# Optimization experiments

Hardware: AMD Instinct MI355X
Metric: run time of the kernel (lower is better)

## Reference

```python
import jax, jax.numpy as jnp
import numpy as np
from jax import lax

B, N, C = 8, 4096, 512
NH, R = 8, 8
HD = C // NH
EPS = 1e-3  # keras LayerNormalization default epsilon


def setup_inputs() -> dict:
    key = jax.random.key(0)
    ks = jax.random.split(key, 8)
    s = 0.02
    x = jax.random.normal(ks[0], (B, N, C), dtype=jnp.float32)
    Wq = jax.random.normal(ks[1], (C, C), dtype=jnp.float32) * s
    Wkv = jax.random.normal(ks[2], (C, 2 * C), dtype=jnp.float32) * s
    conv_w = jax.random.normal(ks[3], (R, R, C, C), dtype=jnp.float32) * s  # HWIO
    gamma = jnp.ones((C,), dtype=jnp.float32)
    beta = jnp.zeros((C,), dtype=jnp.float32)
    Wp = jax.random.normal(ks[4], (C, C), dtype=jnp.float32) * s
    bp = jnp.zeros((C,), dtype=jnp.float32)
    return {"x": x, "Wq": Wq, "Wkv": Wkv, "conv_w": conv_w,
            "gamma": gamma, "beta": beta, "Wp": Wp, "bp": bp}


def reference(x, Wq, Wkv, conv_w, gamma, beta, Wp, bp):
    b, n, c = x.shape
    h = w = int(np.sqrt(n))
    scale = 1.0 / np.sqrt(float(HD))

    # queries: Rearrange 'b n (hd nh) -> b n nh hd' then 'b n nh hd -> b nh n hd'
    q = x @ Wq                                   # [B, N, C]
    q = q.reshape(b, n, HD, NH).transpose(0, 3, 1, 2)  # [B, NH, N, HD]

    # spatial reduction of K/V: strided conv (SAME) + layernorm
    fmap = x.reshape(b, h, w, c)
    fmap = lax.conv_general_dilated(
        fmap, conv_w, window_strides=(R, R), padding="SAME",
        dimension_numbers=("NHWC", "HWIO", "NHWC"))   # [B, h/R, w/R, C]
    m = fmap.shape[1] * fmap.shape[2]
    fmap = fmap.reshape(b, m, c)
    mu = jnp.mean(fmap, axis=-1, keepdims=True)
    var = jnp.var(fmap, axis=-1, keepdims=True)
    fmap = (fmap - mu) * lax.rsqrt(var + EPS) * gamma + beta

    # key/value: Rearrange 'b m (f nh hd) -> b m f nh hd', perm [2,0,3,1,4]
    kv = fmap @ Wkv                              # [B, M, 2C]
    kv = kv.reshape(b, m, 2, NH, HD).transpose(2, 0, 3, 1, 4)  # [2, B, NH, M, HD]
    k, v = kv[0], kv[1]

    attn = jax.nn.softmax(jnp.einsum("bhnd,bhmd->bhnm", q, k) * scale, axis=-1)
    out = jnp.einsum("bhnm,bhmd->bhnd", attn, v)  # [B, NH, N, HD]
    out = out.transpose(0, 2, 1, 3).reshape(b, n, c)  # 'b n h c -> b n (h c)'
    return out @ Wp + bp
```

## Files before the change

### kernel.cpp

```cpp
#include <hip/hip_runtime.h>

typedef unsigned short u16;
typedef __bf16 bf16x8 __attribute__((ext_vector_type(8)));
typedef float floatx4 __attribute__((ext_vector_type(4)));

__device__ __forceinline__ u16 f2bf(float f) {
    unsigned u = __float_as_uint(f);
    u += 0x7fff + ((u >> 16) & 1);
    return (u16)(u >> 16);
}

#define GLOAD_LDS16(g, l) __builtin_amdgcn_global_load_lds( \
    (const __attribute__((address_space(1))) void*)(g),      \
    (__attribute__((address_space(3))) void*)(l), 16, 0, 0)

#define WCONV_STRIDE 32832

__global__ __launch_bounds__(256) void cast_x_kernel(
    const float* __restrict__ x, u16* __restrict__ x_bf)
{
    const int tid = threadIdx.x;
    const size_t base = (size_t)blockIdx.x * 1024 + tid;
    const float4* src = (const float4*)x;
    uint4* dst = (uint4*)x_bf;
    float4 a[4], b[4];
    #pragma unroll
    for (int i = 0; i < 4; ++i) {
        a[i] = src[(base + i * 256) * 2];
        b[i] = src[(base + i * 256) * 2 + 1];
    }
    #pragma unroll
    for (int i = 0; i < 4; ++i) {
        uint4 o;
        o.x = (unsigned)f2bf(a[i].x) | ((unsigned)f2bf(a[i].y) << 16);
        o.y = (unsigned)f2bf(a[i].z) | ((unsigned)f2bf(a[i].w) << 16);
        o.z = (unsigned)f2bf(b[i].x) | ((unsigned)f2bf(b[i].y) << 16);
        o.w = (unsigned)f2bf(b[i].z) | ((unsigned)f2bf(b[i].w) << 16);
        dst[base + i * 256] = o;
    }
}

__global__ __launch_bounds__(256) void prep2_kernel(
    const float* __restrict__ conv_w, u16* __restrict__ WconvT,
    const float* __restrict__ Wq, u16* __restrict__ WqTp,
    const float* __restrict__ Wp, u16* __restrict__ WpT,
    const float* __restrict__ Wkv, u16* __restrict__ WkvT)
{
    int blk = blockIdx.x;
    const int tid = threadIdx.x;
    __shared__ __align__(16) char smem[16896];

    if (blk < 2048) {
        u16 (*T)[66] = (u16(*)[66])smem;
        const int by = blk >> 8;
        const int bx = blk & 255;
        const int c0 = by * 64, k0 = bx * 128;
        const int f = tid & 15, kl = tid >> 4;
        #pragma unroll
        for (int it = 0; it < 8; ++it) {
            int k = kl + it * 16;
            float4 v = *(const float4*)(conv_w + (size_t)(k0 + k) * 512 + c0 + f * 4);
            *(unsigned*)&T[k][f * 4]     = (unsigned)f2bf(v.x) | ((unsigned)f2bf(v.y) << 16);
            *(unsigned*)&T[k][f * 4 + 2] = (unsigned)f2bf(v.z) | ((unsigned)f2bf(v.w) << 16);
        }
        __syncthreads();
        const int cl = tid >> 6, p = tid & 63;
        #pragma unroll
        for (int it = 0; it < 16; ++it) {
            int c = cl + it * 4;
            unsigned lo = T[p * 2][c], hi = T[p * 2 + 1][c];
            *(unsigned*)&WconvT[(size_t)(c0 + c) * WCONV_STRIDE + k0 + p * 2] = lo | (hi << 16);
        }
        return;
    }
    blk -= 2048;

    const float* in; u16* outp; int R, Cn, bx, by; bool perm = false;
    if (blk < 256)      { in = Wq;  outp = WqTp; R = 512; Cn = 512;  bx = blk & 15; by = blk >> 4; perm = true; }
    else if (blk < 512) { blk -= 256; in = Wp;  outp = WpT;  R = 512; Cn = 512;  bx = blk & 15; by = blk >> 4; }
    else                { blk -= 512; in = Wkv; outp = WkvT; R = 512; Cn = 1024; bx = blk & 31; by = blk >> 5; }
    float (*tile)[33] = (float(*)[33])smem;
    const int c0 = bx * 32, r0 = by * 32;
    const int tx = tid & 31, ty = tid >> 5;
    #pragma unroll
    for (int yy = 0; yy < 4; ++yy)
        tile[ty + yy * 8][tx] = in[(size_t)(r0 + ty + yy * 8) * Cn + c0 + tx];
    __syncthreads();
    #pragma unroll
    for (int yy = 0; yy < 4; ++yy) {
        int cc = c0 + ty + yy * 8;
        int np = perm ? ((cc & 7) * 64 + (cc >> 3)) : cc;
        outp[(size_t)np * R + r0 + tx] = f2bf(tile[tx][ty + yy * 8]);
    }
}

template<int MODE, int ASRC>
__global__ __launch_bounds__(256) void gemm_bt(
    const u16* __restrict__ A, const u16* __restrict__ B, float* __restrict__ out,
    int M, int N, int K, int BS, int KC, const float* __restrict__ bias)
{
    __shared__ u16 As[2][128 * 32];
    __shared__ u16 Bs[2][128 * 32];
    const int tid = threadIdx.x;
    const int wv = tid >> 6, lane = tid & 63;
    const int quad = lane >> 4, l15 = lane & 15;

    constexpr int GX = (MODE == 2) ? 8 : 4;
    int id = blockIdx.y * GX + blockIdx.x;
    if (MODE != 0) {
        const int nwg = GX * gridDim.y;
        id = (id & 7) * (nwg >> 3) + (id >> 3);
    }
    const int bm = (id / GX) * 128, bn = (id % GX) * 128;
    const int k0 = blockIdx.z * KC;
    const int wr = wv >> 1, wc = wv & 1;

    floatx4 acc[4][4];
    #pragma unroll
    for (int i = 0; i < 4; ++i)
        #pragma unroll
        for (int j = 0; j < 4; ++j)
            acc[i][j] = (floatx4){0.f, 0.f, 0.f, 0.f};

    for (int kt = 0; kt < KC; kt += 64) {
        const int kk = k0 + kt;
        #pragma unroll
        for (int hf = 0; hf < 2; ++hf) {
            #pragma unroll
            for (int c2 = 0; c2 < 2; ++c2) {
                int idx = ((wv * 2 + c2) * 64 + lane) * 8;
                int row = idx >> 5, col = idx & 31;
                int k = kk + hf * 32 + col;
                if (ASRC == 0) {
                    const u16* ga = A + (size_t)(bm + row) * K + k;
                    GLOAD_LDS16(ga, &As[hf][(wv * 2 + c2) * 512]);
                } else {
                    int p = bm + row;
                    int b = p >> 6, ij = p & 63, ii = ij >> 3, jj = ij & 7;
                    int r12 = k >> 9, r1 = r12 >> 3, r2 = r12 & 7;
                    int n = (ii * 8 + r1) * 64 + jj * 8 + r2;
                    const u16* ga = A + ((size_t)(b * 4096 + n)) * 512 + (k & 511);
                    GLOAD_LDS16(ga, &As[hf][(wv * 2 + c2) * 512]);
                }
                const u16* gb = B + (size_t)(bn + row) * BS + k;
                GLOAD_LDS16(gb, &Bs[hf][(wv * 2 + c2) * 512]);
            }
        }
        __syncthreads();
        #pragma unroll
        for (int ks = 0; ks < 2; ++ks) {
            bf16x8 af[4], bfr[4];
            #pragma unroll
            for (int i = 0; i < 4; ++i)
                af[i] = *(const bf16x8*)&As[ks][(wr * 64 + i * 16 + l15) * 32 + quad * 8];
            #pragma unroll
            for (int j = 0; j < 4; ++j)
                bfr[j] = *(const bf16x8*)&Bs[ks][(wc * 64 + j * 16 + l15) * 32 + quad * 8];
            #pragma unroll
            for (int i = 0; i < 4; ++i)
                #pragma unroll
                for (int j = 0; j < 4; ++j)
                    acc[i][j] = __builtin_amdgcn_mfma_f32_16x16x32_bf16(af[i], bfr[j], acc[i][j], 0, 0, 0);
        }
        __syncthreads();
    }

    #pragma unroll
    for (int i = 0; i < 4; ++i) {
        #pragma unroll
        for (int j = 0; j < 4; ++j) {
            #pragma unroll
            for (int r = 0; r < 4; ++r) {
                int m = bm + wr * 64 + i * 16 + quad * 4 + r;
                int n = bn + wc * 64 + j * 16 + l15;
                float v = acc[i][j][r];
                if (MODE == 0) {
                    ((u16*)out)[(size_t)blockIdx.z * 262144 + (size_t)m * N + n] = f2bf(v);
                } else if (MODE == 1) {
                    int b = m >> 12, nn = m & 4095;
                    int h = n >> 6, d = n & 63;
                    ((u16*)out)[((size_t)((b * 8 + h) * 4096 + nn)) * 64 + d] = f2bf(v);
                } else if (MODE == 2) {
                    int b = m >> 6, mm = m & 63;
                    int f = n >> 9, c = n & 511, h = c >> 6, d = c & 63;
                    size_t idx;
                    if (f == 0) idx = ((size_t)((b * 8 + h) * 64 + mm)) * 64 + d;
                    else        idx = 262144 + ((size_t)((b * 8 + h) * 64 + d)) * 64 + mm;
                    out[idx] = v;
                } else {
                    out[(size_t)m * 512 + n] = v + bias[n];
                }
            }
        }
    }
}

__global__ __launch_bounds__(256) void reduce_ln_bf16(
    const u16* __restrict__ part, u16* __restrict__ out,
    const float* __restrict__ gamma, const float* __restrict__ beta)
{
    int row = blockIdx.x, tid = threadIdx.x;
    const unsigned* base = (const unsigned*)(part + (size_t)row * 512) + tid;
    float2 v = {0.f, 0.f};
    #pragma unroll 8
    for (int z = 0; z < 32; ++z) {
        unsigned u = base[(size_t)z * 131072];
        v.x += __uint_as_float(u << 16);
        v.y += __uint_as_float(u & 0xffff0000u);
    }
    float s = v.x + v.y, ss = v.x * v.x + v.y * v.y;
    #pragma unroll
    for (int off = 32; off > 0; off >>= 1) {
        s  += __shfl_down(s, off);
        ss += __shfl_down(ss, off);
    }
    __shared__ float red[8];
    __shared__ float stats[2];
    int wvi = tid >> 6, lane = tid & 63;
    if (lane == 0) { red[wvi * 2] = s; red[wvi * 2 + 1] = ss; }
    __syncthreads();
    if (tid == 0) {
        float S = red[0] + red[2] + red[4] + red[6];
        float SS = red[1] + red[3] + red[5] + red[7];
        float mean = S * (1.f / 512.f);
        float var = SS * (1.f / 512.f) - mean * mean;
        stats[0] = mean; stats[1] = rsqrtf(var + 1e-3f);
    }
    __syncthreads();
    float mean = stats[0], rstd = stats[1];
    float o0 = (v.x - mean) * rstd * gamma[tid * 2]     + beta[tid * 2];
    float o1 = (v.y - mean) * rstd * gamma[tid * 2 + 1] + beta[tid * 2 + 1];
    unsigned w = (unsigned)f2bf(o0) | ((unsigned)f2bf(o1) << 16);
    *(unsigned*)&out[(size_t)row * 512 + tid * 2] = w;
}

__global__ __launch_bounds__(256) void attn_mfma(
    const u16* __restrict__ qbf, const float* __restrict__ kvf, u16* __restrict__ attn_out)
{
    __shared__ u16 Ksh[64 * 64];
    __shared__ u16 Vt[64 * 64];
    __shared__ u16 Psh[4][32 * 64];
    const int bh = blockIdx.x, qt = blockIdx.y;
    const int tid = threadIdx.x;
    const int wv = tid >> 6, lane = tid & 63;
    const int quad = lane >> 4, l15 = lane & 15;

    {
        const float* kb = kvf + (size_t)bh * 4096;
        const float* vb = kvf + 262144 + (size_t)bh * 4096;
        for (int t = tid; t < 2048; t += 256) {
            float2 a = ((const float2*)kb)[t];
            ((unsigned*)Ksh)[t] = (unsigned)f2bf(a.x) | ((unsigned)f2bf(a.y) << 16);
            float2 b2 = ((const float2*)vb)[t];
            ((unsigned*)Vt)[t] = (unsigned)f2bf(b2.x) | ((unsigned)f2bf(b2.y) << 16);
        }
    }
    __syncthreads();

    const u16* qb = qbf + ((size_t)bh * 4096 + qt * 128 + wv * 32) * 64;
    bf16x8 qf[2][2];
    #pragma unroll
    for (int i = 0; i < 2; ++i)
        #pragma unroll
        for (int ks = 0; ks < 2; ++ks)
            qf[i][ks] = *(const bf16x8*)(qb + (i * 16 + l15) * 64 + ks * 32 + quad * 8);

    floatx4 s[2][4];
    #pragma unroll
    for (int i = 0; i < 2; ++i)
        #pragma unroll
        for (int j = 0; j < 4; ++j)
            s[i][j] = (floatx4){0.f, 0.f, 0.f, 0.f};
    #pragma unroll
    for (int j = 0; j < 4; ++j) {
        #pragma unroll
        for (int ks = 0; ks < 2; ++ks) {
            bf16x8 kf = *(const bf16x8*)&Ksh[(j * 16 + l15) * 64 + ks * 32 + quad * 8];
            #pragma unroll
            for (int i = 0; i < 2; ++i)
                s[i][j] = __builtin_amdgcn_mfma_f32_16x16x32_bf16(qf[i][ks], kf, s[i][j], 0, 0, 0);
        }
    }

    u16* P = Psh[wv];
    float rs[2][4];
    #pragma unroll
    for (int i = 0; i < 2; ++i)
        #pragma unroll
        for (int r = 0; r < 4; ++r) rs[i][r] = 0.f;
    #pragma unroll
    for (int i = 0; i < 2; ++i)
        #pragma unroll
        for (int j = 0; j < 4; ++j)
            #pragma unroll
            for (int r = 0; r < 4; ++r) {
                float e = __expf(s[i][j][r] * 0.125f);
                rs[i][r] += e;
                P[(i * 16 + quad * 4 + r) * 64 + j * 16 + l15] = f2bf(e);
            }
    #pragma unroll
    for (int m = 1; m < 16; m <<= 1)
        #pragma unroll
        for (int i = 0; i < 2; ++i)
            #pragma unroll
            for (int r = 0; r < 4; ++r)
                rs[i][r] += __shfl_xor(rs[i][r], m);
    __syncthreads();

    floatx4 o[2][4];
    #pragma unroll
    for (int i = 0; i < 2; ++i)
        #pragma unroll
        for (int j = 0; j < 4; ++j)
            o[i][j] = (floatx4){0.f, 0.f, 0.f, 0.f};
    #pragma unroll
    for (int ks = 0; ks < 2; ++ks) {
        bf16x8 pf[2];
        #pragma unroll
        for (int i = 0; i < 2; ++i)
            pf[i] = *(const bf16x8*)&P[(i * 16 + l15) * 64 + ks * 32 + quad * 8];
        #pragma unroll
        for (int j = 0; j < 4; ++j) {
            bf16x8 vf = *(const bf16x8*)&Vt[(j * 16 + l15) * 64 + ks * 32 + quad * 8];
            #pragma unroll
            for (int i = 0; i < 2; ++i)
                o[i][j] = __builtin_amdgcn_mfma_f32_16x16x32_bf16(pf[i], vf, o[i][j], 0, 0, 0);
        }
    }

    const int b = bh >> 3, h = bh & 7;
    #pragma unroll
    for (int i = 0; i < 2; ++i) {
        #pragma unroll
        for (int r = 0; r < 4; ++r) {
            float inv = 1.f / rs[i][r];
            int n = qt * 128 + wv * 32 + i * 16 + quad * 4 + r;
            u16* op = attn_out + ((size_t)(b * 4096 + n)) * 512 + h * 64;
            #pragma unroll
            for (int j = 0; j < 4; ++j)
                op[j * 16 + l15] = f2bf(o[i][j][r] * inv);
        }
    }
}

extern "C" void kernel_launch(void* const* d_in, const int* in_sizes, int n_in,
                              void* d_out, int out_size, void* d_ws, size_t ws_size,
                              hipStream_t stream) {
    const float* x      = (const float*)d_in[0];
    const float* Wq     = (const float*)d_in[1];
    const float* Wkv    = (const float*)d_in[2];
    const float* conv_w = (const float*)d_in[3];
    const float* gamma  = (const float*)d_in[4];
    const float* beta   = (const float*)d_in[5];
    const float* Wp     = (const float*)d_in[6];
    const float* bp     = (const float*)d_in[7];
    float* out = (float*)d_out;

    char* w = (char*)d_ws;
    const size_t MB = 1ull << 20;
    u16*   x_bf      = (u16*)(w + 0);
    u16*   WconvT    = (u16*)(w + 32 * MB);
    u16*   WqTp      = (u16*)(w + 66 * MB);
    u16*   WkvT      = (u16*)(w + 67 * MB);
    u16*   WpT       = (u16*)(w + 68 * MB);
    u16*   q_bf      = (u16*)(w + 69 * MB);
    u16*   fmap_part = (u16*)(w + 101 * MB);
    u16*   fmap_ln   = (u16*)(w + 117 * MB);
    float* kv_f      = (float*)(w + 118 * MB);
    u16*   attn_bf   = (u16*)(w + 120 * MB);

    cast_x_kernel<<<2048, 256, 0, stream>>>(x, x_bf);
    prep2_kernel<<<3072, 256, 0, stream>>>(conv_w, WconvT, Wq, WqTp, Wp, WpT, Wkv, WkvT);

    gemm_bt<1, 0><<<dim3(4, 256, 1), 256, 0, stream>>>(x_bf, WqTp, (float*)q_bf, 32768, 512, 512, 512, 512, nullptr);
    gemm_bt<0, 1><<<dim3(4, 4, 32), 256, 0, stream>>>(x_bf, WconvT, (float*)fmap_part, 512, 512, 32768, WCONV_STRIDE, 1024, nullptr);
    reduce_ln_bf16<<<512, 256, 0, stream>>>(fmap_part, fmap_ln, gamma, beta);
    gemm_bt<2, 0><<<dim3(8, 4, 1), 256, 0, stream>>>(fmap_ln, WkvT, kv_f, 512, 1024, 512, 512, 512, nullptr);
    attn_mfma<<<dim3(64, 32), 256, 0, stream>>>(q_bf, kv_f, attn_bf);
    gemm_bt<3, 0><<<dim3(4, 256, 1), 256, 0, stream>>>(attn_bf, WpT, out, 32768, 512, 512, 512, 512, bp);
}
```

Measured before the change: 317.4 us.

## Merge prep kernels, co-launch Q and conv GEMMs, double-buffer GEMM K loop

Folds the x cast into the weight-prep kernel so it is one launch. The Q-projection GEMM and the strided-conv split-K GEMM now run as one fused launch with a block-index dispatch. The GEMM body now uses a ping-pong double-buffered 32-wide K loop, so global-to-LDS loads for the next step overlap the MFMA compute on the current one. This removes launch gaps and tail underutilisation, at the cost of finer-grained syncs and more complex block scheduling.

```diff
diff --git a/kernel.cpp b/kernel.cpp
--- a/kernel.cpp
+++ b/kernel.cpp
@@ -16,31 +16,8 @@
 
 #define WCONV_STRIDE 32832
 
-__global__ __launch_bounds__(256) void cast_x_kernel(
-    const float* __restrict__ x, u16* __restrict__ x_bf)
-{
-    const int tid = threadIdx.x;
-    const size_t base = (size_t)blockIdx.x * 1024 + tid;
-    const float4* src = (const float4*)x;
-    uint4* dst = (uint4*)x_bf;
-    float4 a[4], b[4];
-    #pragma unroll
-    for (int i = 0; i < 4; ++i) {
-        a[i] = src[(base + i * 256) * 2];
-        b[i] = src[(base + i * 256) * 2 + 1];
-    }
-    #pragma unroll
-    for (int i = 0; i < 4; ++i) {
-        uint4 o;
-        o.x = (unsigned)f2bf(a[i].x) | ((unsigned)f2bf(a[i].y) << 16);
-        o.y = (unsigned)f2bf(a[i].z) | ((unsigned)f2bf(a[i].w) << 16);
-        o.z = (unsigned)f2bf(b[i].x) | ((unsigned)f2bf(b[i].y) << 16);
-        o.w = (unsigned)f2bf(b[i].z) | ((unsigned)f2bf(b[i].w) << 16);
-        dst[base + i * 256] = o;
-    }
-}
-
-__global__ __launch_bounds__(256) void prep2_kernel(
+__global__ __launch_bounds__(256) void prep_kernel(
+    const float* __restrict__ x, u16* __restrict__ x_bf,
     const float* __restrict__ conv_w, u16* __restrict__ WconvT,
     const float* __restrict__ Wq, u16* __restrict__ WqTp,
     const float* __restrict__ Wp, u16* __restrict__ WpT,
@@ -48,6 +25,30 @@
 {
     int blk = blockIdx.x;
     const int tid = threadIdx.x;
+
+    if (blk < 2048) {
+        const size_t base = (size_t)blk * 1024 + tid;
+        const float4* src = (const float4*)x;
+        uint4* dst = (uint4*)x_bf;
+        float4 a[4], b[4];
+        #pragma unroll
+        for (int i = 0; i < 4; ++i) {
+            a[i] = src[(base + i * 256) * 2];
+            b[i] = src[(base + i * 256) * 2 + 1];
+        }
+        #pragma unroll
+        for (int i = 0; i < 4; ++i) {
+            uint4 o;
+            o.x = (unsigned)f2bf(a[i].x) | ((unsigned)f2bf(a[i].y) << 16);
+            o.y = (unsigned)f2bf(a[i].z) | ((unsigned)f2bf(a[i].w) << 16);
+            o.z = (unsigned)f2bf(b[i].x) | ((unsigned)f2bf(b[i].y) << 16);
+            o.w = (unsigned)f2bf(b[i].z) | ((unsigned)f2bf(b[i].w) << 16);
+            dst[base + i * 256] = o;
+        }
+        return;
+    }
+    blk -= 2048;
+
     __shared__ __align__(16) char smem[16896];
 
     if (blk < 2048) {
@@ -95,24 +96,17 @@
 }
 
 template<int MODE, int ASRC>
-__global__ __launch_bounds__(256) void gemm_bt(
+__device__ __forceinline__ void gemm_body(
     const u16* __restrict__ A, const u16* __restrict__ B, float* __restrict__ out,
-    int M, int N, int K, int BS, int KC, const float* __restrict__ bias)
-{
-    __shared__ u16 As[2][128 * 32];
-    __shared__ u16 Bs[2][128 * 32];
+    int M, int N, int K, int BS, int KC, const float* __restrict__ bias,
+    int id, int zz, u16 (*As)[4096], u16 (*Bs)[4096])
+{
     const int tid = threadIdx.x;
     const int wv = tid >> 6, lane = tid & 63;
     const int quad = lane >> 4, l15 = lane & 15;
-
     constexpr int GX = (MODE == 2) ? 8 : 4;
-    int id = blockIdx.y * GX + blockIdx.x;
-    if (MODE != 0) {
-        const int nwg = GX * gridDim.y;
-        id = (id & 7) * (nwg >> 3) + (id >> 3);
-    }
     const int bm = (id / GX) * 128, bn = (id % GX) * 128;
-    const int k0 = blockIdx.z * KC;
+    const int k0 = zz * KC;
     const int wr = wv >> 1, wc = wv & 1;
 
     floatx4 acc[4][4];
@@ -122,46 +116,50 @@
         for (int j = 0; j < 4; ++j)
             acc[i][j] = (floatx4){0.f, 0.f, 0.f, 0.f};
 
-    for (int kt = 0; kt < KC; kt += 64) {
-        const int kk = k0 + kt;
-        #pragma unroll
-        for (int hf = 0; hf < 2; ++hf) {
-            #pragma unroll
-            for (int c2 = 0; c2 < 2; ++c2) {
-                int idx = ((wv * 2 + c2) * 64 + lane) * 8;
-                int row = idx >> 5, col = idx & 31;
-                int k = kk + hf * 32 + col;
-                if (ASRC == 0) {
-                    const u16* ga = A + (size_t)(bm + row) * K + k;
-                    GLOAD_LDS16(ga, &As[hf][(wv * 2 + c2) * 512]);
-                } else {
-                    int p = bm + row;
-                    int b = p >> 6, ij = p & 63, ii = ij >> 3, jj = ij & 7;
-                    int r12 = k >> 9, r1 = r12 >> 3, r2 = r12 & 7;
-                    int n = (ii * 8 + r1) * 64 + jj * 8 + r2;
-                    const u16* ga = A + ((size_t)(b * 4096 + n)) * 512 + (k & 511);
-                    GLOAD_LDS16(ga, &As[hf][(wv * 2 + c2) * 512]);
-                }
-                const u16* gb = B + (size_t)(bn + row) * BS + k;
-                GLOAD_LDS16(gb, &Bs[hf][(wv * 2 + c2) * 512]);
+    auto stage = [&](int step, int buf) {
+        const int kk = k0 + (step << 5);
+        #pragma unroll
+        for (int c2 = 0; c2 < 2; ++c2) {
+            const int chunk = wv * 2 + c2;
+            const int idx = (chunk * 64 + lane) * 8;
+            const int row = idx >> 5, col = idx & 31;
+            const int k = kk + col;
+            if (ASRC == 0) {
+                GLOAD_LDS16(A + (size_t)(bm + row) * K + k, &As[buf][chunk * 512]);
+            } else {
+                int p = bm + row;
+                int b = p >> 6, ij = p & 63, ii = ij >> 3, jj = ij & 7;
+                int r12 = k >> 9, r1 = r12 >> 3, r2 = r12 & 7;
+                int n = (ii * 8 + r1) * 64 + jj * 8 + r2;
+                GLOAD_LDS16(A + ((size_t)(b * 4096 + n)) * 512 + (k & 511), &As[buf][chunk * 512]);
             }
-        }
+            GLOAD_LDS16(B + (size_t)(bn + row) * BS + k, &Bs[buf][chunk * 512]);
+        }
+    };
+    auto compute = [&](int buf) {
+        bf16x8 af[4], bfr[4];
+        #pragma unroll
+        for (int i = 0; i < 4; ++i)
+            af[i] = *(const bf16x8*)&As[buf][(wr * 64 + i * 16 + l15) * 32 + quad * 8];
+        #pragma unroll
+        for (int j = 0; j < 4; ++j)
+            bfr[j] = *(const bf16x8*)&Bs[buf][(wc * 64 + j * 16 + l15) * 32 + quad * 8];
+        #pragma unroll
+        for (int i = 0; i < 4; ++i)
+            #pragma unroll
+            for (int j = 0; j < 4; ++j)
+                acc[i][j] = __builtin_amdgcn_mfma_f32_16x16x32_bf16(af[i], bfr[j], acc[i][j], 0, 0, 0);
+    };
+
+    const int nsteps = KC >> 5;
+    stage(0, 0);
+    __syncthreads();
+    for (int step = 0; step < nsteps; step += 2) {
+        stage(step + 1, 1);
+        compute(0);
         __syncthreads();
-        #pragma unroll
-        for (int ks = 0; ks < 2; ++ks) {
-            bf16x8 af[4], bfr[4];
-            #pragma unroll
-            for (int i = 0; i < 4; ++i)
-                af[i] = *(const bf16x8*)&As[ks][(wr * 64 + i * 16 + l15) * 32 + quad * 8];
-            #pragma unroll
-            for (int j = 0; j < 4; ++j)
-                bfr[j] = *(const bf16x8*)&Bs[ks][(wc * 64 + j * 16 + l15) * 32 + quad * 8];
-            #pragma unroll
-            for (int i = 0; i < 4; ++i)
-                #pragma unroll
-                for (int j = 0; j < 4; ++j)
-                    acc[i][j] = __builtin_amdgcn_mfma_f32_16x16x32_bf16(af[i], bfr[j], acc[i][j], 0, 0, 0);
-        }
+        if (step + 2 < nsteps) stage(step + 2, 0);
+        compute(1);
         __syncthreads();
     }
 
@@ -175,7 +173,7 @@
                 int n = bn + wc * 64 + j * 16 + l15;
                 float v = acc[i][j][r];
                 if (MODE == 0) {
-                    ((u16*)out)[(size_t)blockIdx.z * 262144 + (size_t)m * N + n] = f2bf(v);
+                    ((u16*)out)[(size_t)zz * 262144 + (size_t)m * N + n] = f2bf(v);
                 } else if (MODE == 1) {
                     int b = m >> 12, nn = m & 4095;
                     int h = n >> 6, d = n & 63;
@@ -195,6 +193,37 @@
     }
 }
 
+template<int MODE, int ASRC>
+__global__ __launch_bounds__(256) void gemm_bt(
+    const u16* __restrict__ A, const u16* __restrict__ B, float* __restrict__ out,
+    int M, int N, int K, int BS, int KC, const float* __restrict__ bias)
+{
+    __shared__ u16 As[2][4096], Bs[2][4096];
+    int id = blockIdx.x;
+    if (MODE != 0) {
+        const int nwg = gridDim.x;
+        id = (id & 7) * (nwg >> 3) + (id >> 3);
+    }
+    gemm_body<MODE, ASRC>(A, B, out, M, N, K, BS, KC, bias, id, blockIdx.z, As, Bs);
+}
+
+__global__ __launch_bounds__(256) void gemm_qconv(
+    const u16* __restrict__ x_bf, const u16* __restrict__ WconvT, u16* __restrict__ fmap_part,
+    const u16* __restrict__ WqTp, u16* __restrict__ q_bf)
+{
+    __shared__ u16 As[2][4096], Bs[2][4096];
+    const int blk = blockIdx.x;
+    if (blk < 512) {
+        gemm_body<0, 1>(x_bf, WconvT, (float*)fmap_part, 512, 512, 32768, WCONV_STRIDE, 1024,
+                        nullptr, blk & 15, blk >> 4, As, Bs);
+    } else {
+        int id = blk - 512;
+        id = (id & 7) * 128 + (id >> 3);
+        gemm_body<1, 0>(x_bf, WqTp, (float*)q_bf, 32768, 512, 512, 512, 512,
+                        nullptr, id, 0, As, Bs);
+    }
+}
+
 __global__ __launch_bounds__(256) void reduce_ln_bf16(
     const u16* __restrict__ part, u16* __restrict__ out,
     const float* __restrict__ gamma, const float* __restrict__ beta)
@@ -369,13 +398,12 @@
     float* kv_f      = (float*)(w + 118 * MB);
     u16*   attn_bf   = (u16*)(w + 120 * MB);
 
-    cast_x_kernel<<<2048, 256, 0, stream>>>(x, x_bf);
-    prep2_kernel<<<3072, 256, 0, stream>>>(conv_w, WconvT, Wq, WqTp, Wp, WpT, Wkv, WkvT);
-
-    gemm_bt<1, 0><<<dim3(4, 256, 1), 256, 0, stream>>>(x_bf, WqTp, (float*)q_bf, 32768, 512, 512, 512, 512, nullptr);
-    gemm_bt<0, 1><<<dim3(4, 4, 32), 256, 0, stream>>>(x_bf, WconvT, (float*)fmap_part, 512, 512, 32768, WCONV_STRIDE, 1024, nullptr);
+    prep_kernel<<<5120, 256, 0, stream>>>(x, x_bf, conv_w, WconvT, Wq, WqTp, Wp, WpT, Wkv, WkvT);
+
+    gemm_qconv<<<1536, 256, 0, stream>>>(x_bf, WconvT, fmap_part, WqTp, q_bf);
+
     reduce_ln_bf16<<<512, 256, 0, stream>>>(fmap_part, fmap_ln, gamma, beta);
-    gemm_bt<2, 0><<<dim3(8, 4, 1), 256, 0, stream>>>(fmap_ln, WkvT, kv_f, 512, 1024, 512, 512, 512, nullptr);
+    gemm_bt<2, 0><<<32, 256, 0, stream>>>(fmap_ln, WkvT, kv_f, 512, 1024, 512, 512, 512, nullptr);
     attn_mfma<<<dim3(64, 32), 256, 0, stream>>>(q_bf, kv_f, attn_bf);
-    gemm_bt<3, 0><<<dim3(4, 256, 1), 256, 0, stream>>>(attn_bf, WpT, out, 32768, 512, 512, 512, 512, bp);
-}
+    gemm_bt<3, 0><<<1024, 256, 0, stream>>>(attn_bf, WpT, out, 32768, 512, 512, 512, 512, bp);
+}
```

Result: no change. 314.0 us (-1.1%).
